# Kernel tuning notes

Measured on AMD Instinct MI355X. Metric: run time of the kernel, lower is better.

Reference implementation:

```python
import jax, jax.numpy as jnp
import numpy as np

DIM = 96
EPS = 1e-5

def setup_inputs() -> dict:
    key = jax.random.key(0)
    k1, k2, k3, k4 = jax.random.split(key, 4)
    x = jax.random.normal(k1, (2, DIM, 32, 64, 64), dtype=jnp.float32)
    # LayerNorm(8*dim) params and Linear(8*dim -> 2*dim, bias=False) weight
    gamma = jnp.ones((8 * DIM,), dtype=jnp.float32)
    beta = jnp.zeros((8 * DIM,), dtype=jnp.float32)
    w_red = jax.random.normal(k2, (8 * DIM, 2 * DIM), dtype=jnp.float32) * (1.0 / np.sqrt(8 * DIM))
    return {"x": x, "gamma": gamma, "beta": beta, "w_red": w_red}


def _patch_merge(x, gamma, beta, w_red):
    B, C, D, H, W = x.shape
    # pad trailing spatial dims to even (static shapes -> python ifs are fine)
    if (D % 2) or (H % 2) or (W % 2):
        x = jnp.pad(x, ((0, 0), (0, 0), (0, D % 2), (0, H % 2), (0, W % 2)))
    x = jnp.transpose(x, (0, 2, 3, 4, 1))  # B, D, H, W, C
    # gather the 8 octant sub-lattices and concat on channel
    parts = [x[:, d::2, h::2, w::2, :]
             for d in (0, 1) for h in (0, 1) for w in (0, 1)]
    # torch order: x0..x7 indexed by (d,h,w) bits with d slowest -> matches loop order
    y = jnp.concatenate(parts, axis=-1)  # B, D/2, H/2, W/2, 8C
    # LayerNorm over last dim
    mu = jnp.mean(y, axis=-1, keepdims=True)
    var = jnp.mean(jnp.square(y - mu), axis=-1, keepdims=True)
    y = (y - mu) * jax.lax.rsqrt(var + EPS) * gamma + beta
    # Linear 8C -> 2C, no bias
    y = jnp.einsum('bdhwc,co->bdhwo', y, w_red)
    return jnp.transpose(y, (0, 4, 1, 2, 3))  # B, 2C, D/2, H/2, W/2


def reference(x, gamma, beta, w_red):
    return _patch_merge(x, gamma, beta, w_red)
```

## Files before the change

kernel.cpp:

```cpp
#include <hip/hip_runtime.h>

typedef __attribute__((ext_vector_type(8))) short short8;
typedef __attribute__((ext_vector_type(4))) float float4v;

__device__ __forceinline__ unsigned short f2bf(float f) {
  unsigned int u = __float_as_uint(f);
  u += 0x7fffu + ((u >> 16) & 1u);
  return (unsigned short)(u >> 16);
}
__device__ __forceinline__ float bf2f(unsigned short h) {
  return __uint_as_float(((unsigned int)h) << 16);
}

__global__ __launch_bounds__(256)
void prep_kernel(const float* __restrict__ w_red, const float* __restrict__ gamma,
                 const float* __restrict__ beta, unsigned short* __restrict__ w_bf,
                 float* __restrict__ colsum, float* __restrict__ bias) {
  const int n = blockIdx.x;
  const int t = threadIdx.x;
  float cs = 0.f, bs = 0.f;
#pragma unroll
  for (int j = 0; j < 3; ++j) {
    int kp = j * 256 + t;
    int ko = (kp & 7) * 96 + (kp >> 3);
    float w = w_red[(size_t)ko * 192 + n];
    unsigned short v = f2bf(gamma[ko] * w);
    w_bf[(size_t)n * 768 + kp] = v;
    cs += bf2f(v);
    bs += beta[ko] * w;
  }
#pragma unroll
  for (int off = 1; off < 64; off <<= 1) {
    cs += __shfl_xor(cs, off, 64);
    bs += __shfl_xor(bs, off, 64);
  }
  __shared__ float red[2][4];
  const int wave = t >> 6;
  if ((t & 63) == 0) { red[0][wave] = cs; red[1][wave] = bs; }
  __syncthreads();
  if (t == 0) {
    colsum[n] = red[0][0] + red[0][1] + red[0][2] + red[0][3];
    bias[n]   = red[1][0] + red[1][1] + red[1][2] + red[1][3];
  }
}

__global__ __launch_bounds__(256, 3)
void pm_kernel(const float* __restrict__ x, const unsigned short* __restrict__ w_bf,
               const float* __restrict__ colsum, const float* __restrict__ bias,
               float* __restrict__ out) {
  __shared__ __align__(16) unsigned short Y[32][776];
  __shared__ float4 part4[4][16];
  __shared__ float smu[32], srs[32];

  const int tid = threadIdx.x;
  const int bid = blockIdx.x;
  const int b  = bid >> 9;
  const int dz = (bid >> 5) & 15;
  const int hy = bid & 31;

  const float* xb = x + (size_t)b * 12582912u + (size_t)dz * 8192u + (size_t)hy * 128u;

  const int r0 = tid >> 4;
  const int c0 = r0 >> 2;
  const int di = (r0 >> 1) & 1;
  const int hi = r0 & 1;
  const int w0 = (tid & 15) << 2;
  const float* xp = xb + (size_t)c0 * 131072u + di * 4096 + hi * 64 + w0;

  float4 v[24];
#pragma unroll
  for (int it = 0; it < 24; ++it)
    v[it] = *(const float4*)(xp + (size_t)it * 524288u);

  const int lane = tid & 63;
  const int wave = tid >> 6;
  const int lrow = lane & 15;
  const int lq   = lane >> 4;
  const unsigned short* wrow[3];
#pragma unroll
  for (int t3 = 0; t3 < 3; ++t3)
    wrow[t3] = w_bf + (size_t)((wave * 3 + t3) * 16 + lrow) * 768 + lq * 8;
  short8 b0[3], b1[3];
#pragma unroll
  for (int t3 = 0; t3 < 3; ++t3) b0[t3] = *(const short8*)(wrow[t3]);
#pragma unroll
  for (int t3 = 0; t3 < 3; ++t3) b1[t3] = *(const short8*)(wrow[t3] + 32);

  const int wx0 = (tid & 15) << 1;
  const int k00 = c0 * 8 + di * 4 + hi * 2;
  float sum0 = 0.f, sq0 = 0.f, sum1 = 0.f, sq1 = 0.f;
#pragma unroll
  for (int it = 0; it < 24; ++it) {
    float4 vv = v[it];
    unsigned int p01 = (unsigned int)f2bf(vv.x) | ((unsigned int)f2bf(vv.y) << 16);
    unsigned int p23 = (unsigned int)f2bf(vv.z) | ((unsigned int)f2bf(vv.w) << 16);
    int k0 = it * 32 + k00;
    *(unsigned int*)&Y[wx0][k0]     = p01;
    *(unsigned int*)&Y[wx0 + 1][k0] = p23;
    sum0 += vv.x + vv.y;  sq0 += vv.x * vv.x + vv.y * vv.y;
    sum1 += vv.z + vv.w;  sq1 += vv.z * vv.z + vv.w * vv.w;
  }
#pragma unroll
  for (int off = 16; off < 64; off <<= 1) {
    sum0 += __shfl_xor(sum0, off, 64);  sq0 += __shfl_xor(sq0, off, 64);
    sum1 += __shfl_xor(sum1, off, 64);  sq1 += __shfl_xor(sq1, off, 64);
  }
  if (lane < 16) part4[wave][lane] = make_float4(sum0, sq0, sum1, sq1);
  __syncthreads();

  if (tid < 32) {
    int sp = tid >> 1, odd = tid & 1;
    float s = 0.f, q = 0.f;
#pragma unroll
    for (int w = 0; w < 4; ++w) {
      float4 p = part4[w][sp];
      s += odd ? p.z : p.x;
      q += odd ? p.w : p.y;
    }
    float mu  = s * (1.f / 768.f);
    float var = q * (1.f / 768.f) - mu * mu;
    smu[tid] = mu;
    srs[tid] = rsqrtf(var + 1e-5f);
  }

  float4v acc[2][3];
#pragma unroll
  for (int i2 = 0; i2 < 2; ++i2)
#pragma unroll
    for (int j2 = 0; j2 < 3; ++j2)
#pragma unroll
      for (int r = 0; r < 4; ++r) acc[i2][j2][r] = 0.f;

  for (int kc = 0; kc < 24; ++kc) {
    int kn = (kc + 2 <= 23) ? kc + 2 : 23;
    short8 b2[3];
#pragma unroll
    for (int t3 = 0; t3 < 3; ++t3) b2[t3] = *(const short8*)(wrow[t3] + kn * 32);
    short8 a0 = *(const short8*)&Y[lrow][kc * 32 + lq * 8];
    short8 a1 = *(const short8*)&Y[16 + lrow][kc * 32 + lq * 8];
#pragma unroll
    for (int t3 = 0; t3 < 3; ++t3) {
      acc[0][t3] = __builtin_amdgcn_mfma_f32_16x16x32_bf16(a0, b0[t3], acc[0][t3], 0, 0, 0);
      acc[1][t3] = __builtin_amdgcn_mfma_f32_16x16x32_bf16(a1, b0[t3], acc[1][t3], 0, 0, 0);
    }
#pragma unroll
    for (int t3 = 0; t3 < 3; ++t3) { b0[t3] = b1[t3]; b1[t3] = b2[t3]; }
  }

  float cs_n[3], bi_n[3];
#pragma unroll
  for (int t3 = 0; t3 < 3; ++t3) {
    int ng = (wave * 3 + t3) * 16 + lrow;
    cs_n[t3] = colsum[ng];
    bi_n[t3] = bias[ng];
  }

  __syncthreads();
  float* Cs = (float*)&Y[0][0];
#pragma unroll
  for (int t3 = 0; t3 < 3; ++t3) {
    int ng = (wave * 3 + t3) * 16 + lrow;
#pragma unroll
    for (int mt = 0; mt < 2; ++mt)
#pragma unroll
      for (int r = 0; r < 4; ++r) {
        int m = mt * 16 + lq * 4 + r;
        float vv = srs[m] * (acc[mt][t3][r] - smu[m] * cs_n[t3]) + bi_n[t3];
        Cs[ng * 40 + m] = vv;
      }
  }
  __syncthreads();

  float* ob = out + (size_t)b * 3145728u + (size_t)dz * 1024u + (size_t)hy * 32u;
#pragma unroll
  for (int it = 0; it < 6; ++it) {
    int idx4 = it * 256 + tid;
    int o  = idx4 >> 3;
    int wq = idx4 & 7;
    float4 vv = *(const float4*)&Cs[o * 40 + wq * 4];
    *(float4*)(ob + (size_t)o * 16384u + wq * 4) = vv;
  }
}

extern "C" void kernel_launch(void* const* d_in, const int* in_sizes, int n_in,
                              void* d_out, int out_size, void* d_ws, size_t ws_size,
                              hipStream_t stream) {
  const float* x     = (const float*)d_in[0];
  const float* gamma = (const float*)d_in[1];
  const float* beta  = (const float*)d_in[2];
  const float* w_red = (const float*)d_in[3];
  float* out = (float*)d_out;

  unsigned short* w_bf = (unsigned short*)d_ws;
  float* colsum = (float*)((char*)d_ws + 294912);
  float* bias   = colsum + 192;

  prep_kernel<<<dim3(192), dim3(256), 0, stream>>>(w_red, gamma, beta, w_bf, colsum, bias);
  pm_kernel<<<dim3(1024), dim3(256), 0, stream>>>(x, w_bf, colsum, bias, out);
}
```

Measured before the change: 190.1 us.

## Stage input via direct global-to-LDS loads and halve the per-block tile

Input x tiles are now loaded with global_load_lds straight into shared memory instead of through 24 float4 registers per thread. Each block handles half the W extent (16 output positions), so the grid doubles to 2048 blocks and each wave issues a single MFMA row tile. This is meant to cut register pressure and put more memory requests in flight. The cost is a 48KB LDS staging buffer, a launch bound lowered to 2 blocks per SU, and twice the weight-fragment reads from global memory across blocks.

```diff
diff --git a/kernel.cpp b/kernel.cpp
--- a/kernel.cpp
+++ b/kernel.cpp
@@ -11,6 +11,11 @@
 __device__ __forceinline__ float bf2f(unsigned short h) {
   return __uint_as_float(((unsigned int)h) << 16);
 }
+
+#define GLOBAL_LOAD_LDS16(gptr, lptr)                                          \
+  __builtin_amdgcn_global_load_lds(                                            \
+      (const __attribute__((address_space(1))) unsigned int*)(gptr),           \
+      (__attribute__((address_space(3))) unsigned int*)(lptr), 16, 0, 0)
 
 __global__ __launch_bounds__(256)
 void prep_kernel(const float* __restrict__ w_red, const float* __restrict__ gamma,
@@ -44,76 +49,73 @@
   }
 }
 
-__global__ __launch_bounds__(256, 3)
+__global__ __launch_bounds__(256, 2)
 void pm_kernel(const float* __restrict__ x, const unsigned short* __restrict__ w_bf,
                const float* __restrict__ colsum, const float* __restrict__ bias,
                float* __restrict__ out) {
-  __shared__ __align__(16) unsigned short Y[32][776];
-  __shared__ float4 part4[4][16];
-  __shared__ float smu[32], srs[32];
+  __shared__ __align__(16) float LDSX[12288];
+  __shared__ __align__(16) unsigned short Y[16][792];
+  __shared__ float4 part[4][8];
+  __shared__ float smu[16], srs[16];
 
   const int tid = threadIdx.x;
   const int bid = blockIdx.x;
-  const int b  = bid >> 9;
-  const int dz = (bid >> 5) & 15;
-  const int hy = bid & 31;
-
-  const float* xb = x + (size_t)b * 12582912u + (size_t)dz * 8192u + (size_t)hy * 128u;
-
-  const int r0 = tid >> 4;
-  const int c0 = r0 >> 2;
-  const int di = (r0 >> 1) & 1;
-  const int hi = r0 & 1;
-  const int w0 = (tid & 15) << 2;
-  const float* xp = xb + (size_t)c0 * 131072u + di * 4096 + hi * 64 + w0;
-
-  float4 v[24];
-#pragma unroll
-  for (int it = 0; it < 24; ++it)
-    v[it] = *(const float4*)(xp + (size_t)it * 524288u);
-
-  const int lane = tid & 63;
+  const int b  = bid >> 10;
+  const int dz = (bid >> 6) & 15;
+  const int hy = (bid >> 1) & 31;
+  const int wh = bid & 1;
+
+  const float* xb = x + (size_t)b * 12582912u + (size_t)dz * 8192u
+                      + (size_t)hy * 128u + wh * 32;
+
+  const int rr   = tid >> 3;
+  const int seg  = tid & 7;
   const int wave = tid >> 6;
-  const int lrow = lane & 15;
-  const int lq   = lane >> 4;
-  const unsigned short* wrow[3];
-#pragma unroll
-  for (int t3 = 0; t3 < 3; ++t3)
-    wrow[t3] = w_bf + (size_t)((wave * 3 + t3) * 16 + lrow) * 768 + lq * 8;
-  short8 b0[3], b1[3];
-#pragma unroll
-  for (int t3 = 0; t3 < 3; ++t3) b0[t3] = *(const short8*)(wrow[t3]);
-#pragma unroll
-  for (int t3 = 0; t3 < 3; ++t3) b1[t3] = *(const short8*)(wrow[t3] + 32);
-
-  const int wx0 = (tid & 15) << 1;
-  const int k00 = c0 * 8 + di * 4 + hi * 2;
+
+#pragma unroll
+  for (int it = 0; it < 12; ++it) {
+    int r  = it * 32 + rr;
+    int c  = r >> 2;
+    int di = (r >> 1) & 1;
+    int hi = r & 1;
+    const float* gp = xb + (size_t)c * 131072u + di * 4096 + hi * 64 + seg * 4;
+    float* lp = &LDSX[it * 1024 + wave * 256];
+    GLOBAL_LOAD_LDS16(gp, lp);
+  }
+  __syncthreads();
+
+  const int wx0 = seg * 2;
   float sum0 = 0.f, sq0 = 0.f, sum1 = 0.f, sq1 = 0.f;
 #pragma unroll
-  for (int it = 0; it < 24; ++it) {
-    float4 vv = v[it];
+  for (int it = 0; it < 12; ++it) {
+    int r  = it * 32 + rr;
+    int c  = r >> 2;
+    int di = (r >> 1) & 1;
+    int hi = r & 1;
+    float4 vv = *(const float4*)&LDSX[it * 1024 + rr * 32 + seg * 4];
+    int k0 = c * 8 + di * 4 + hi * 2;
     unsigned int p01 = (unsigned int)f2bf(vv.x) | ((unsigned int)f2bf(vv.y) << 16);
     unsigned int p23 = (unsigned int)f2bf(vv.z) | ((unsigned int)f2bf(vv.w) << 16);
-    int k0 = it * 32 + k00;
     *(unsigned int*)&Y[wx0][k0]     = p01;
     *(unsigned int*)&Y[wx0 + 1][k0] = p23;
     sum0 += vv.x + vv.y;  sq0 += vv.x * vv.x + vv.y * vv.y;
     sum1 += vv.z + vv.w;  sq1 += vv.z * vv.z + vv.w * vv.w;
   }
-#pragma unroll
-  for (int off = 16; off < 64; off <<= 1) {
+  const int lane = tid & 63;
+#pragma unroll
+  for (int off = 8; off < 64; off <<= 1) {
     sum0 += __shfl_xor(sum0, off, 64);  sq0 += __shfl_xor(sq0, off, 64);
     sum1 += __shfl_xor(sum1, off, 64);  sq1 += __shfl_xor(sq1, off, 64);
   }
-  if (lane < 16) part4[wave][lane] = make_float4(sum0, sq0, sum1, sq1);
-  __syncthreads();
-
-  if (tid < 32) {
-    int sp = tid >> 1, odd = tid & 1;
+  if (lane < 8) part[wave][lane] = make_float4(sum0, sq0, sum1, sq1);
+  __syncthreads();
+
+  if (tid < 16) {
+    int sg = tid >> 1, odd = tid & 1;
     float s = 0.f, q = 0.f;
 #pragma unroll
     for (int w = 0; w < 4; ++w) {
-      float4 p = part4[w][sp];
+      float4 p = part[w][sg];
       s += odd ? p.z : p.x;
       q += odd ? p.w : p.y;
     }
@@ -123,26 +125,34 @@
     srs[tid] = rsqrtf(var + 1e-5f);
   }
 
-  float4v acc[2][3];
-#pragma unroll
-  for (int i2 = 0; i2 < 2; ++i2)
-#pragma unroll
-    for (int j2 = 0; j2 < 3; ++j2)
-#pragma unroll
-      for (int r = 0; r < 4; ++r) acc[i2][j2][r] = 0.f;
+  const int lrow = lane & 15;
+  const int lq   = lane >> 4;
+  const unsigned short* wrow[3];
+#pragma unroll
+  for (int t3 = 0; t3 < 3; ++t3)
+    wrow[t3] = w_bf + (size_t)((wave * 3 + t3) * 16 + lrow) * 768 + lq * 8;
+
+  short8 b0[3], b1[3];
+#pragma unroll
+  for (int t3 = 0; t3 < 3; ++t3) b0[t3] = *(const short8*)(wrow[t3]);
+#pragma unroll
+  for (int t3 = 0; t3 < 3; ++t3) b1[t3] = *(const short8*)(wrow[t3] + 32);
+
+  float4v acc[3];
+#pragma unroll
+  for (int t3 = 0; t3 < 3; ++t3)
+#pragma unroll
+    for (int r = 0; r < 4; ++r) acc[t3][r] = 0.f;
 
   for (int kc = 0; kc < 24; ++kc) {
     int kn = (kc + 2 <= 23) ? kc + 2 : 23;
     short8 b2[3];
 #pragma unroll
     for (int t3 = 0; t3 < 3; ++t3) b2[t3] = *(const short8*)(wrow[t3] + kn * 32);
-    short8 a0 = *(const short8*)&Y[lrow][kc * 32 + lq * 8];
-    short8 a1 = *(const short8*)&Y[16 + lrow][kc * 32 + lq * 8];
-#pragma unroll
-    for (int t3 = 0; t3 < 3; ++t3) {
-      acc[0][t3] = __builtin_amdgcn_mfma_f32_16x16x32_bf16(a0, b0[t3], acc[0][t3], 0, 0, 0);
-      acc[1][t3] = __builtin_amdgcn_mfma_f32_16x16x32_bf16(a1, b0[t3], acc[1][t3], 0, 0, 0);
-    }
+    short8 a = *(const short8*)&Y[lrow][kc * 32 + lq * 8];
+#pragma unroll
+    for (int t3 = 0; t3 < 3; ++t3)
+      acc[t3] = __builtin_amdgcn_mfma_f32_16x16x32_bf16(a, b0[t3], acc[t3], 0, 0, 0);
 #pragma unroll
     for (int t3 = 0; t3 < 3; ++t3) { b0[t3] = b1[t3]; b1[t3] = b2[t3]; }
   }
@@ -161,23 +171,22 @@
   for (int t3 = 0; t3 < 3; ++t3) {
     int ng = (wave * 3 + t3) * 16 + lrow;
 #pragma unroll
-    for (int mt = 0; mt < 2; ++mt)
-#pragma unroll
-      for (int r = 0; r < 4; ++r) {
-        int m = mt * 16 + lq * 4 + r;
-        float vv = srs[m] * (acc[mt][t3][r] - smu[m] * cs_n[t3]) + bi_n[t3];
-        Cs[ng * 40 + m] = vv;
-      }
-  }
-  __syncthreads();
-
-  float* ob = out + (size_t)b * 3145728u + (size_t)dz * 1024u + (size_t)hy * 32u;
-#pragma unroll
-  for (int it = 0; it < 6; ++it) {
-    int idx4 = it * 256 + tid;
-    int o  = idx4 >> 3;
-    int wq = idx4 & 7;
-    float4 vv = *(const float4*)&Cs[o * 40 + wq * 4];
+    for (int r = 0; r < 4; ++r) {
+      int m = lq * 4 + r;
+      float vv = srs[m] * (acc[t3][r] - smu[m] * cs_n[t3]) + bi_n[t3];
+      Cs[ng * 20 + m] = vv;
+    }
+  }
+  __syncthreads();
+
+  float* ob = out + (size_t)b * 3145728u + (size_t)dz * 1024u
+                  + (size_t)hy * 32u + wh * 16;
+#pragma unroll
+  for (int it = 0; it < 3; ++it) {
+    int idx = it * 256 + tid;
+    int o  = idx >> 2;
+    int wq = idx & 3;
+    float4 vv = *(const float4*)&Cs[o * 20 + wq * 4];
     *(float4*)(ob + (size_t)o * 16384u + wq * 4) = vv;
   }
 }
@@ -196,5 +205,5 @@
   float* bias   = colsum + 192;
 
   prep_kernel<<<dim3(192), dim3(256), 0, stream>>>(w_red, gamma, beta, w_bf, colsum, bias);
-  pm_kernel<<<dim3(1024), dim3(256), 0, stream>>>(x, w_bf, colsum, bias, out);
-}
+  pm_kernel<<<dim3(2048), dim3(256), 0, stream>>>(x, w_bf, colsum, bias, out);
+}
```

After: 222.9 us. 1.17x slower.
